# Kernel optimization log

Hardware: AMD Instinct MI355X
Metric: run time of the kernel (lower is better)

## Reference

```python
import jax, jax.numpy as jnp
import numpy as np

GROUP = 128  # K-rows per scale group, matching (in_features+127)//128 scale rows


def setup_inputs() -> dict:
    key = jax.random.key(0)
    k1, k2, k3, k4, k5, k6 = jax.random.split(key, 6)
    M, K, N = 512, 8192, 8192
    x = jax.random.normal(k1, (M, K), dtype=jnp.float32)
    # packed 4-bit codes: each byte holds two nibble indices along N -> [K, N//2]
    packed = jax.random.randint(k2, (K, N // 2), 0, 256, dtype=jnp.int32)
    grid = jax.random.normal(k3, (16,), dtype=jnp.float32)  # 2^bits codebook entries
    scales = jax.random.uniform(k4, (K // GROUP, N), dtype=jnp.float32)
    su = jax.random.normal(k5, (K,), dtype=jnp.float32)
    sv = jax.random.normal(k6, (N,), dtype=jnp.float32)
    return {"x": x, "packed": packed, "grid": grid, "scales": scales, "su": su, "sv": sv}


def _dequant(packed, grid, scales, su, sv):
    # Unpack two 4-bit indices per byte (low nibble first) along N.
    K = packed.shape[0]
    N = packed.shape[1] * 2
    low = packed & 0xF
    high = (packed >> 4) & 0xF
    idx = jnp.stack([low, high], axis=-1).reshape(K, N)  # [K, N] codes in [0,16)
    w = grid[idx]                                        # codebook lookup
    # per-group (128 K-rows) x per-output-column scales
    w = (w.reshape(K // GROUP, GROUP, N) * scales[:, None, :]).reshape(K, N)
    # input/output sign/scale vectors
    return w * su[:, None] * sv[None, :]


def reference(x, packed, grid, scales, su, sv):
    W = _dequant(packed, grid, scales, su, sv)  # [K, N]
    return x @ W                                 # [M, N]
```

## Files before the change

### kernel.cpp

```cpp
#include <hip/hip_runtime.h>


typedef __attribute__((ext_vector_type(8))) short short8;
typedef __attribute__((ext_vector_type(4))) float f32x4;

__device__ __forceinline__ unsigned short f2bf(float f) {
  unsigned int u = __builtin_bit_cast(unsigned int, f);
  u += 0x7FFFu + ((u >> 16) & 1u);
  return (unsigned short)(u >> 16);
}

__device__ __forceinline__ void gld16(const void* g, void* l) {
  __builtin_amdgcn_global_load_lds(
      (__attribute__((address_space(1))) void*)(g),
      (__attribute__((address_space(3))) void*)(l), 16, 0, 0);
}

__global__ __launch_bounds__(256) void zero_out(float4* __restrict__ p, int n4) {
  int i = blockIdx.x * 256 + threadIdx.x;
  int stride = gridDim.x * 256;
  for (; i < n4; i += stride) p[i] = float4{0.f, 0.f, 0.f, 0.f};
}

__global__ __launch_bounds__(256) void convert_x_su(
    const float* __restrict__ x, const float* __restrict__ su,
    unsigned short* __restrict__ xp, int K) {
  int k = blockIdx.x * 2048 + threadIdx.x * 8;
  size_t i = (size_t)blockIdx.y * K + k;
  float4 x0 = *(const float4*)(x + i);
  float4 x1 = *(const float4*)(x + i + 4);
  float4 s0 = *(const float4*)(su + k);
  float4 s1 = *(const float4*)(su + k + 4);
  unsigned int r0 = f2bf(x0.x * s0.x) | ((unsigned int)f2bf(x0.y * s0.y) << 16);
  unsigned int r1 = f2bf(x0.z * s0.z) | ((unsigned int)f2bf(x0.w * s0.w) << 16);
  unsigned int r2 = f2bf(x1.x * s1.x) | ((unsigned int)f2bf(x1.y * s1.y) << 16);
  unsigned int r3 = f2bf(x1.z * s1.z) | ((unsigned int)f2bf(x1.w * s1.w) << 16);
  uint4 o; o.x = r0; o.y = r1; o.z = r2; o.w = r3;
  *(uint4*)(xp + i) = o;
}

__global__ __launch_bounds__(256) void dequant_wt(
    const int* __restrict__ packed, const float* __restrict__ gridv,
    const float* __restrict__ scales, const float* __restrict__ sv,
    unsigned short* __restrict__ Wt, int K, int N) {
  __shared__ float sGp[32];
  __shared__ float sA[128];
  __shared__ unsigned short sW[128 * 128];

  int t = threadIdx.x;
  int n0 = blockIdx.x * 128;
  int k0 = blockIdx.y * 128;
  int g = k0 >> 7;
  if (t < 16) sGp[t * 2] = gridv[t];
  if (t < 128) sA[t] = scales[(size_t)g * N + n0 + t] * sv[n0 + t];
  __syncthreads();

  int c = t & 63;
  int w = t >> 6;
  size_t rs = (size_t)(N >> 1);
  const int* p = packed + (size_t)(k0 + w * 32) * rs + (n0 >> 1) + c;
  int pv[32];
#pragma unroll
  for (int j = 0; j < 32; ++j) pv[j] = p[(size_t)j * rs];

  float aLo = sA[2 * c], aHi = sA[2 * c + 1];
  unsigned int w0[16], w1[16];
#pragma unroll
  for (int q = 0; q < 16; ++q) {
    int va = pv[2 * q], vb = pv[2 * q + 1];
    w0[q] = (unsigned int)f2bf(sGp[(va & 15) * 2] * aLo) |
            ((unsigned int)f2bf(sGp[(vb & 15) * 2] * aLo) << 16);
    w1[q] = (unsigned int)f2bf(sGp[((va >> 4) & 15) * 2] * aHi) |
            ((unsigned int)f2bf(sGp[((vb >> 4) & 15) * 2] * aHi) << 16);
  }
  int nA = 2 * c, nB = 2 * c + 1;
#pragma unroll
  for (int q = 0; q < 4; ++q) {
    int ch = w * 4 + q;
    uint4 va; va.x = w0[4*q]; va.y = w0[4*q+1]; va.z = w0[4*q+2]; va.w = w0[4*q+3];
    uint4 vb; vb.x = w1[4*q]; vb.y = w1[4*q+1]; vb.z = w1[4*q+2]; vb.w = w1[4*q+3];
    *(uint4*)&sW[nA * 128 + ((ch ^ (nA & 15)) << 3)] = va;
    *(uint4*)&sW[nB * 128 + ((ch ^ (nB & 15)) << 3)] = vb;
  }
  __syncthreads();

#pragma unroll
  for (int ps = 0; ps < 8; ++ps) {
    int n = ps * 16 + (t >> 4);
    int ch = t & 15;
    uint4 v = *(const uint4*)&sW[n * 128 + ((ch ^ (n & 15)) << 3)];
    *(uint4*)(Wt + (size_t)(n0 + n) * K + k0 + ch * 8) = v;
  }
}

#define BM 128
#define BN 128
#define BK 64
#define KSLICES 4

__global__ __launch_bounds__(256, 3) void gemm_xw(
    const unsigned short* __restrict__ A,
    const unsigned short* __restrict__ B,
    float* __restrict__ C, int M, int N, int K) {
  __shared__ unsigned short As[BM * BK];
  __shared__ unsigned short Bs[BN * BK];

  int t = threadIdx.x;
  int l = t & 63;
  int w = t >> 6;
  int wr = w >> 1, wc = w & 1;
  size_t m0 = (size_t)blockIdx.y * BM;
  size_t n0 = (size_t)blockIdx.x * BN;
  int kbeg = blockIdx.z * (K / KSLICES);
  int kend = kbeg + K / KSLICES;

  const unsigned short* Ag = A + m0 * K;
  const unsigned short* Bg = B + n0 * K;

  int srow = t >> 3;
  int sch = t & 7;

  int lr = l & 15;
  int lh = l >> 4;

  f32x4 acc[4][4] = {};

  for (int k0 = kbeg; k0 < kend; k0 += BK) {
#pragma unroll
    for (int r = 0; r < 4; ++r) {
      int row = r * 32 + srow;
      int sc = (sch ^ (row & 7)) * 8;
      gld16(Ag + (size_t)row * K + k0 + sc, &As[row * BK + sch * 8]);
    }
#pragma unroll
    for (int r = 0; r < 4; ++r) {
      int row = r * 32 + srow;
      int sc = (sch ^ (row & 7)) * 8;
      gld16(Bg + (size_t)row * K + k0 + sc, &Bs[row * BK + sch * 8]);
    }
    __syncthreads();

#pragma unroll
    for (int kh = 0; kh < 2; ++kh) {
      short8 a[4], b[4];
      int sk = kh * 4 + lh;
#pragma unroll
      for (int i = 0; i < 4; ++i) {
        int row = wr * 64 + i * 16 + lr;
        a[i] = *(const short8*)&As[row * BK + ((sk ^ (row & 7)) << 3)];
      }
#pragma unroll
      for (int j = 0; j < 4; ++j) {
        int row = wc * 64 + j * 16 + lr;
        b[j] = *(const short8*)&Bs[row * BK + ((sk ^ (row & 7)) << 3)];
      }
#pragma unroll
      for (int i = 0; i < 4; ++i)
#pragma unroll
        for (int j = 0; j < 4; ++j)
          acc[i][j] = __builtin_amdgcn_mfma_f32_16x16x32_bf16(a[i], b[j], acc[i][j], 0, 0, 0);
    }
    __syncthreads();
  }

#pragma unroll
  for (int i = 0; i < 4; ++i)
#pragma unroll
    for (int j = 0; j < 4; ++j) {
      size_t row = m0 + wr * 64 + i * 16 + lh * 4;
      size_t col = n0 + wc * 64 + j * 16 + lr;
#pragma unroll
      for (int r = 0; r < 4; ++r)
        atomicAdd(&C[(row + r) * N + col], acc[i][j][r]);
    }
}

extern "C" void kernel_launch(void* const* d_in, const int* in_sizes, int n_in,
                              void* d_out, int out_size, void* d_ws, size_t ws_size,
                              hipStream_t stream) {
  const float* x      = (const float*)d_in[0];
  const int*   packed = (const int*)d_in[1];
  const float* gridv  = (const float*)d_in[2];
  const float* scales = (const float*)d_in[3];
  const float* su     = (const float*)d_in[4];
  const float* sv     = (const float*)d_in[5];
  float* out = (float*)d_out;

  int K = in_sizes[4];
  int N = in_sizes[5];
  int M = in_sizes[0] / K;

  unsigned short* xp = (unsigned short*)d_ws;
  unsigned short* Wt = xp + (size_t)M * K;

  zero_out<<<1024, 256, 0, stream>>>((float4*)out, (M * N) / 4);
  convert_x_su<<<dim3(K / 2048, M), 256, 0, stream>>>(x, su, xp, K);
  dequant_wt<<<dim3(N / 128, K / 128), 256, 0, stream>>>(packed, gridv, scales, sv, Wt, K, N);
  gemm_xw<<<dim3(N / BN, M / BM, KSLICES), 256, 0, stream>>>(xp, Wt, out, M, N, K);
}
```

Before: 363.5 us.

## Fuse weight dequantization into GEMM B-tile staging with register prefetch

Removes the standalone dequant kernel that wrote a bf16 transposed weight matrix to workspace. The GEMM now loads packed 4-bit codes, decodes them through an LDS codebook with per-group scales times sv, and writes bf16 B tiles directly into shared memory. The next tile's packed codes are prefetched into registers during the MFMA loop. A block-index swizzle groups M-blocks that share the same N-tile. This avoids the full-size bf16 weight write and re-read, but each of the four M-blocks now re-dequantizes the same weights, which adds ALU work and register pressure to the GEMM loop.

```diff
diff --git a/kernel.cpp b/kernel.cpp
--- a/kernel.cpp
+++ b/kernel.cpp
@@ -39,106 +39,104 @@
   *(uint4*)(xp + i) = o;
 }
 
-__global__ __launch_bounds__(256) void dequant_wt(
-    const int* __restrict__ packed, const float* __restrict__ gridv,
-    const float* __restrict__ scales, const float* __restrict__ sv,
-    unsigned short* __restrict__ Wt, int K, int N) {
-  __shared__ float sGp[32];
-  __shared__ float sA[128];
-  __shared__ unsigned short sW[128 * 128];
-
-  int t = threadIdx.x;
-  int n0 = blockIdx.x * 128;
-  int k0 = blockIdx.y * 128;
-  int g = k0 >> 7;
-  if (t < 16) sGp[t * 2] = gridv[t];
-  if (t < 128) sA[t] = scales[(size_t)g * N + n0 + t] * sv[n0 + t];
-  __syncthreads();
-
-  int c = t & 63;
-  int w = t >> 6;
-  size_t rs = (size_t)(N >> 1);
-  const int* p = packed + (size_t)(k0 + w * 32) * rs + (n0 >> 1) + c;
-  int pv[32];
-#pragma unroll
-  for (int j = 0; j < 32; ++j) pv[j] = p[(size_t)j * rs];
-
-  float aLo = sA[2 * c], aHi = sA[2 * c + 1];
-  unsigned int w0[16], w1[16];
-#pragma unroll
-  for (int q = 0; q < 16; ++q) {
-    int va = pv[2 * q], vb = pv[2 * q + 1];
-    w0[q] = (unsigned int)f2bf(sGp[(va & 15) * 2] * aLo) |
-            ((unsigned int)f2bf(sGp[(vb & 15) * 2] * aLo) << 16);
-    w1[q] = (unsigned int)f2bf(sGp[((va >> 4) & 15) * 2] * aHi) |
-            ((unsigned int)f2bf(sGp[((vb >> 4) & 15) * 2] * aHi) << 16);
-  }
-  int nA = 2 * c, nB = 2 * c + 1;
-#pragma unroll
-  for (int q = 0; q < 4; ++q) {
-    int ch = w * 4 + q;
-    uint4 va; va.x = w0[4*q]; va.y = w0[4*q+1]; va.z = w0[4*q+2]; va.w = w0[4*q+3];
-    uint4 vb; vb.x = w1[4*q]; vb.y = w1[4*q+1]; vb.z = w1[4*q+2]; vb.w = w1[4*q+3];
-    *(uint4*)&sW[nA * 128 + ((ch ^ (nA & 15)) << 3)] = va;
-    *(uint4*)&sW[nB * 128 + ((ch ^ (nB & 15)) << 3)] = vb;
-  }
-  __syncthreads();
-
-#pragma unroll
-  for (int ps = 0; ps < 8; ++ps) {
-    int n = ps * 16 + (t >> 4);
-    int ch = t & 15;
-    uint4 v = *(const uint4*)&sW[n * 128 + ((ch ^ (n & 15)) << 3)];
-    *(uint4*)(Wt + (size_t)(n0 + n) * K + k0 + ch * 8) = v;
-  }
-}
-
 #define BM 128
 #define BN 128
 #define BK 64
 #define KSLICES 4
 
-__global__ __launch_bounds__(256, 3) void gemm_xw(
+__global__ __launch_bounds__(256, 3) void gemm_fused(
     const unsigned short* __restrict__ A,
-    const unsigned short* __restrict__ B,
+    const int* __restrict__ packed,
+    const float* __restrict__ gridv,
+    const float* __restrict__ scales,
+    const float* __restrict__ sv,
     float* __restrict__ C, int M, int N, int K) {
   __shared__ unsigned short As[BM * BK];
   __shared__ unsigned short Bs[BN * BK];
+  __shared__ float sS[16 * 128];
+  __shared__ float sGp[32];
 
   int t = threadIdx.x;
   int l = t & 63;
   int w = t >> 6;
+
+  int nwg = gridDim.x;
+  int bid = blockIdx.x;
+  int swz = (bid & 7) * (nwg >> 3) + (bid >> 3);
+  int mblocks = M >> 7;
+  int mb = swz % mblocks;
+  int nb = swz / mblocks;
+  size_t m0 = (size_t)mb * BM;
+  size_t n0 = (size_t)nb * BN;
+  int kbeg = blockIdx.y * (K / KSLICES);
+  int kend = kbeg + K / KSLICES;
+
+  if (t < 16) { float g = gridv[t]; sGp[t * 2] = g; sGp[t * 2 + 1] = g; }
+  int g0 = kbeg >> 7;
+  for (int i = t; i < 16 * 128; i += 256) {
+    int g = i >> 7, n = i & 127;
+    sS[i] = scales[(size_t)(g0 + g) * N + n0 + n] * sv[n0 + n];
+  }
+  __syncthreads();
+
+  const unsigned short* Ag = A + m0 * K;
+  size_t rs = (size_t)(N >> 1);
+  int c = l;
+  int kq = w;
+  const int* pbase = packed + (n0 >> 1) + c + (size_t)(kq * 16) * rs;
+  const float* lut = &sGp[l & 1];
+
+  int srow = t >> 3, sch = t & 7;
+  int lr = l & 15, lh = l >> 4;
   int wr = w >> 1, wc = w & 1;
-  size_t m0 = (size_t)blockIdx.y * BM;
-  size_t n0 = (size_t)blockIdx.x * BN;
-  int kbeg = blockIdx.z * (K / KSLICES);
-  int kend = kbeg + K / KSLICES;
-
-  const unsigned short* Ag = A + m0 * K;
-  const unsigned short* Bg = B + n0 * K;
-
-  int srow = t >> 3;
-  int sch = t & 7;
-
-  int lr = l & 15;
-  int lh = l >> 4;
+  int nA = 2 * c, nB = 2 * c + 1;
 
   f32x4 acc[4][4] = {};
 
+  int pv[16];
+  {
+    const int* p = pbase + (size_t)kbeg * rs;
+#pragma unroll
+    for (int j = 0; j < 16; ++j) pv[j] = p[(size_t)j * rs];
+  }
+
   for (int k0 = kbeg; k0 < kend; k0 += BK) {
+    int gl = (k0 - kbeg) >> 7;
+    float2 a2 = *(const float2*)&sS[gl * 128 + nA];
+#pragma unroll
+    for (int q = 0; q < 2; ++q) {
+      int ch = kq * 2 + q;
+      uint4 va, vb;
+      unsigned int* pa = (unsigned int*)&va;
+      unsigned int* pbv = (unsigned int*)&vb;
+#pragma unroll
+      for (int d = 0; d < 4; ++d) {
+        int v0 = pv[q * 8 + 2 * d], v1 = pv[q * 8 + 2 * d + 1];
+        float w00 = lut[(v0 & 15) << 1];
+        float w01 = lut[(v1 & 15) << 1];
+        float w10 = lut[((v0 >> 4) & 15) << 1];
+        float w11 = lut[((v1 >> 4) & 15) << 1];
+        pa[d]  = (unsigned int)f2bf(w00 * a2.x) | ((unsigned int)f2bf(w01 * a2.x) << 16);
+        pbv[d] = (unsigned int)f2bf(w10 * a2.y) | ((unsigned int)f2bf(w11 * a2.y) << 16);
+      }
+      *(uint4*)&Bs[nA * BK + ((ch ^ (nA & 7)) << 3)] = va;
+      *(uint4*)&Bs[nB * BK + ((ch ^ (nB & 7)) << 3)] = vb;
+    }
+
 #pragma unroll
     for (int r = 0; r < 4; ++r) {
       int row = r * 32 + srow;
       int sc = (sch ^ (row & 7)) * 8;
       gld16(Ag + (size_t)row * K + k0 + sc, &As[row * BK + sch * 8]);
     }
-#pragma unroll
-    for (int r = 0; r < 4; ++r) {
-      int row = r * 32 + srow;
-      int sc = (sch ^ (row & 7)) * 8;
-      gld16(Bg + (size_t)row * K + k0 + sc, &Bs[row * BK + sch * 8]);
-    }
     __syncthreads();
+
+    int pvn[16] = {};
+    if (k0 + BK < kend) {
+      const int* p = pbase + (size_t)(k0 + BK) * rs;
+#pragma unroll
+      for (int j = 0; j < 16; ++j) pvn[j] = p[(size_t)j * rs];
+    }
 
 #pragma unroll
     for (int kh = 0; kh < 2; ++kh) {
@@ -161,6 +159,9 @@
           acc[i][j] = __builtin_amdgcn_mfma_f32_16x16x32_bf16(a[i], b[j], acc[i][j], 0, 0, 0);
     }
     __syncthreads();
+
+#pragma unroll
+    for (int j = 0; j < 16; ++j) pv[j] = pvn[j];
   }
 
 #pragma unroll
@@ -191,10 +192,10 @@
   int M = in_sizes[0] / K;
 
   unsigned short* xp = (unsigned short*)d_ws;
-  unsigned short* Wt = xp + (size_t)M * K;
 
   zero_out<<<1024, 256, 0, stream>>>((float4*)out, (M * N) / 4);
   convert_x_su<<<dim3(K / 2048, M), 256, 0, stream>>>(x, su, xp, K);
-  dequant_wt<<<dim3(N / 128, K / 128), 256, 0, stream>>>(packed, gridv, scales, sv, Wt, K, N);
-  gemm_xw<<<dim3(N / BN, M / BM, KSLICES), 256, 0, stream>>>(xp, Wt, out, M, N, K);
-}
+  int nwg = (N / BN) * (M / BM);
+  gemm_fused<<<dim3(nwg, KSLICES), 256, 0, stream>>>(xp, packed, gridv, scales, sv,
+                                                     out, M, N, K);
+}
```

Result: faster. 326.9 us (-10.1%).
